# Kernel tuning notes

Hardware: AMD Instinct MI355X
Metric: run time of the kernel (lower is better)

Reference implementation:

```python
import jax, jax.numpy as jnp
import numpy as np

N0, N1, N2 = 100000, 25000, 6250
E0, E1, E2 = 600000, 150000, 40000
K = 6
NUM_CLASSES = 10


def setup_inputs() -> dict:
    key = jax.random.key(0)
    ks = jax.random.split(key, 20)
    inp = {
        "pos": jax.random.normal(ks[0], (N0, 3), dtype=jnp.float32),
        "edge_index0": jax.random.randint(ks[1], (2, E0), 0, N0, dtype=jnp.int32),
        "edge_index1": jax.random.randint(ks[2], (2, E1), 0, N1, dtype=jnp.int32),
        "edge_index2": jax.random.randint(ks[3], (2, E2), 0, N2, dtype=jnp.int32),
        "d0_rows": jax.random.randint(ks[4], (N0,), 0, N1, dtype=jnp.int32),
        "d0_cols": jax.random.randint(ks[5], (N0,), 0, N0, dtype=jnp.int32),
        "d0_vals": jax.random.uniform(ks[6], (N0,), dtype=jnp.float32),
        "d1_rows": jax.random.randint(ks[7], (N1,), 0, N2, dtype=jnp.int32),
        "d1_cols": jax.random.randint(ks[8], (N1,), 0, N1, dtype=jnp.int32),
        "d1_vals": jax.random.uniform(ks[9], (N1,), dtype=jnp.float32),
        "W0": jax.random.normal(ks[10], (K, 3, 32), dtype=jnp.float32) * 0.1,
        "b0": jax.random.normal(ks[11], (32,), dtype=jnp.float32) * 0.1,
        "W1": jax.random.normal(ks[12], (K, 32, 64), dtype=jnp.float32) * 0.1,
        "b1": jax.random.normal(ks[13], (64,), dtype=jnp.float32) * 0.1,
        "W2": jax.random.normal(ks[14], (K, 64, 128), dtype=jnp.float32) * 0.1,
        "b2": jax.random.normal(ks[15], (128,), dtype=jnp.float32) * 0.1,
        "lin_w": jax.random.normal(ks[16], (NUM_CLASSES, N2 * 128), dtype=jnp.float32) * 0.01,
        "lin_b": jax.random.normal(ks[17], (NUM_CLASSES,), dtype=jnp.float32) * 0.1,
    }
    return inp


def _cheb_edge_weights(row, col, n):
    # PyG get_laplacian(sym) followed by 2L/lambda_max - I with lambda_max=2:
    # diagonal becomes 0, off-diagonal weight = -deg^{-1/2}[row] * deg^{-1/2}[col]
    deg = jax.ops.segment_sum(jnp.ones(row.shape[0], jnp.float32), row, num_segments=n)
    dinv = jnp.where(deg > 0, 1.0 / jnp.sqrt(deg), 0.0)
    return -dinv[row] * dinv[col]


def _cheb_conv(x, edge_index, W, b, n):
    # Chebyshev recurrence: Tx0 = x, Tx1 = L_hat x, Tx_k = 2 L_hat Tx_{k-1} - Tx_{k-2}
    row, col = edge_index[0], edge_index[1]
    w = _cheb_edge_weights(row, col, n)

    def prop(z):  # [n, C] -> [n, C] scatter-gather over edges
        return jax.ops.segment_sum(w[:, None] * z[col], row, num_segments=n)

    Tx0 = x
    out = Tx0 @ W[0]
    Tx1 = prop(x)
    out = out + Tx1 @ W[1]
    for k in range(2, W.shape[0]):
        Tx2 = 2.0 * prop(Tx1) - Tx0
        out = out + Tx2 @ W[k]
        Tx0, Tx1 = Tx1, Tx2
    return out + b


def _pool(x, rows, cols, vals, n_out):
    # torch.sparse.mm(D, x) with D given in COO form
    return jax.ops.segment_sum(vals[:, None] * x[cols], rows, num_segments=n_out)


def reference(pos, edge_index0, edge_index1, edge_index2,
              d0_rows, d0_cols, d0_vals, d1_rows, d1_cols, d1_vals,
              W0, b0, W1, b1, W2, b2, lin_w, lin_b):
    x = jax.nn.relu(_cheb_conv(pos, edge_index0, W0, b0, N0))
    x = _pool(x, d0_rows, d0_cols, d0_vals, N1)
    x = jax.nn.relu(_cheb_conv(x, edge_index1, W1, b1, N1))
    x = _pool(x, d1_rows, d1_cols, d1_vals, N2)
    x = _cheb_conv(x, edge_index2, W2, b2, N2)  # no ReLU on last conv
    Z = lin_w @ x.reshape(-1) + lin_b
    return Z
```

## Files before the change

kernel.cpp:

```cpp
#include <hip/hip_runtime.h>


#define TPB 256
#define NB   318
#define BCAP 8192
#define EPB  4096
#define TXS  800000LL

static inline int gs(long long n) { return (int)((n + TPB - 1) / TPB); }

struct Desc5 {
    const int* rows[5];
    const int* cols[5];
    const float* vals[5];
    int eoff[6];
    int doff[5];
};


__global__ void k_binA(Desc5 d, int* __restrict__ gbcnt, int2* __restrict__ binrec,
                       int Etot) {
    __shared__ int2 srec[EPB];
    __shared__ unsigned short sbuck[EPB];
    __shared__ int scnt[NB], sbase[NB], slcur[NB];
    int tid = threadIdx.x;
    int e0 = blockIdx.x * EPB;
    int ne = min(EPB, Etot - e0);
    for (int b = tid; b < NB; b += 256) scnt[b] = 0;
    __syncthreads();
    for (int i = tid; i < ne; i += 256) {
        int e = e0 + i;
        int s = 0;
        while (e >= d.eoff[s + 1]) ++s;
        int le = e - d.eoff[s];
        int grow = d.doff[s] + d.rows[s][le];
        int col = d.cols[s][le];
        int vb = (s >= 3) ? __float_as_int(d.vals[s][le]) : 0;
        int b = grow >> 9;
        srec[i] = make_int2(((grow & 511) << 17) | col, vb);
        sbuck[i] = (unsigned short)b;
        atomicAdd(&scnt[b], 1);
    }
    __syncthreads();
    for (int b = tid; b < NB; b += 256) {
        sbase[b] = scnt[b] > 0 ? atomicAdd(&gbcnt[b], scnt[b]) : 0;
        slcur[b] = 0;
    }
    __syncthreads();
    for (int i = tid; i < ne; i += 256) {
        int b = sbuck[i];
        int off = atomicAdd(&slcur[b], 1);
        binrec[(long long)b * BCAP + sbase[b] + off] = srec[i];
    }
}

__global__ void k_bscan(const int* __restrict__ gbcnt, int* __restrict__ gbbase) {
    int lane = threadIdx.x;
    int carry = 0;
    for (int base = 0; base < NB; base += 64) {
        int i = base + lane;
        int v = (i < NB) ? gbcnt[i] : 0;
        int s = v;
#pragma unroll
        for (int off = 1; off < 64; off <<= 1) {
            int t = __shfl_up(s, off, 64);
            if (lane >= off) s += t;
        }
        if (i < NB) gbbase[i] = carry + s - v;
        carry += __shfl(s, 63, 64);
    }
}

__global__ void k_B1(const int* __restrict__ gbcnt, const int* __restrict__ gbbase,
                     const int2* __restrict__ binrec, int* __restrict__ rowptr,
                     float* __restrict__ dinv, int ntot, int ndinv, int Etot) {
    __shared__ int cnt[512], lexcl[512], wsum[4];
    int bucket = blockIdx.x, tid = threadIdx.x;
    int ne = gbcnt[bucket];
    const int2* br = binrec + (long long)bucket * BCAP;
    cnt[2 * tid] = 0; cnt[2 * tid + 1] = 0;
    __syncthreads();
    for (int i = tid; i < ne; i += 256)
        atomicAdd(&cnt[br[i].x >> 17], 1);
    __syncthreads();
    int c0 = cnt[2 * tid], c1 = cnt[2 * tid + 1], p = c0 + c1;
    int lane = tid & 63, wid = tid >> 6;
    int s = p;
#pragma unroll
    for (int off = 1; off < 64; off <<= 1) {
        int t = __shfl_up(s, off, 64);
        if (lane >= off) s += t;
    }
    if (lane == 63) wsum[wid] = s;
    __syncthreads();
    int add = 0;
    for (int w = 0; w < wid; ++w) add += wsum[w];
    int ep = add + s - p;
    lexcl[2 * tid] = ep; lexcl[2 * tid + 1] = ep + c0;
    __syncthreads();
    int base = gbbase[bucket];
    int row0 = bucket << 9;
    int nrows = min(512, ntot - row0);
    for (int lr = tid; lr < nrows; lr += 256) {
        int grow = row0 + lr;
        rowptr[grow] = base + lexcl[lr];
        if (grow < ndinv) {
            int c = cnt[lr];
            dinv[grow] = c > 0 ? 1.0f / sqrtf((float)c) : 0.f;
        }
    }
    if (bucket == 0 && tid == 0) rowptr[ntot] = Etot;
}

__global__ void k_B2(const int* __restrict__ gbcnt, const int2* __restrict__ binrec,
                     const int* __restrict__ rowptr, const float* __restrict__ dinv,
                     int2* __restrict__ rec, int ntot) {
    __shared__ int lbase[512], lcur[512];
    int bucket = blockIdx.x, tid = threadIdx.x;
    int row0 = bucket << 9;
    for (int i = tid; i < 512; i += 256) {
        int grow = row0 + i;
        lbase[i] = (grow < ntot) ? rowptr[grow] : 0;
        lcur[i] = 0;
    }
    __syncthreads();
    int ne = gbcnt[bucket];
    const int2* br = binrec + (long long)bucket * BCAP;
    for (int i = tid; i < ne; i += 256) {
        int2 r = br[i];
        int lr = r.x >> 17, col = r.x & 0x1FFFF;
        int grow = row0 + lr;
        int pos = lbase[lr] + atomicAdd(&lcur[lr], 1);
        float wv;
        if (grow < 100000)      wv = dinv[col];
        else if (grow < 125000) wv = dinv[100000 + col];
        else if (grow < 131250) wv = dinv[125000 + col];
        else                    wv = __int_as_float(r.y);
        rec[pos] = make_int2(col, __float_as_int(wv));
    }
}

__global__ void k_pad4(const float* __restrict__ pos, float4* __restrict__ dst, int n) {
    int i = blockIdx.x * blockDim.x + threadIdx.x;
    if (i < n) dst[i] = make_float4(pos[3 * i], pos[3 * i + 1], pos[3 * i + 2], 0.f);
}


__global__ void k_sprop_c4(const int* __restrict__ rowptr, const int2* __restrict__ rec,
                           const float* __restrict__ dinv, const float* __restrict__ src,
                           const float* __restrict__ prev, float* __restrict__ dst,
                           int n, int mode) {
    int r = blockIdx.x * blockDim.x + threadIdx.x;
    if (r >= n) return;
    int s0 = rowptr[r], s1 = rowptr[r + 1];
    float4 a0 = make_float4(0.f, 0.f, 0.f, 0.f);
    float4 a1 = a0, a2 = a0, a3 = a0;
    int j = s0;
    if ((j & 1) && j < s1) {
        int2 rr = rec[j];
        float w = __int_as_float(rr.y);
        float4 s = *(const float4*)(src + (long long)rr.x * 4);
        a0.x += w * s.x; a0.y += w * s.y; a0.z += w * s.z; a0.w += w * s.w;
        ++j;
    }
    for (; j + 4 <= s1; j += 4) {
        int4 q0 = *(const int4*)(rec + j);
        int4 q1 = *(const int4*)(rec + j + 2);
        float w0 = __int_as_float(q0.y), w1 = __int_as_float(q0.w);
        float w2 = __int_as_float(q1.y), w3 = __int_as_float(q1.w);
        float4 s0v = *(const float4*)(src + (long long)q0.x * 4);
        float4 s1v = *(const float4*)(src + (long long)q0.z * 4);
        float4 s2v = *(const float4*)(src + (long long)q1.x * 4);
        float4 s3v = *(const float4*)(src + (long long)q1.z * 4);
        a0.x += w0 * s0v.x; a0.y += w0 * s0v.y; a0.z += w0 * s0v.z; a0.w += w0 * s0v.w;
        a1.x += w1 * s1v.x; a1.y += w1 * s1v.y; a1.z += w1 * s1v.z; a1.w += w1 * s1v.w;
        a2.x += w2 * s2v.x; a2.y += w2 * s2v.y; a2.z += w2 * s2v.z; a2.w += w2 * s2v.w;
        a3.x += w3 * s3v.x; a3.y += w3 * s3v.y; a3.z += w3 * s3v.z; a3.w += w3 * s3v.w;
    }
    if (j + 2 <= s1) {
        int4 q = *(const int4*)(rec + j);
        float wa = __int_as_float(q.y), wb = __int_as_float(q.w);
        float4 sa = *(const float4*)(src + (long long)q.x * 4);
        float4 sb = *(const float4*)(src + (long long)q.z * 4);
        a0.x += wa * sa.x; a0.y += wa * sa.y; a0.z += wa * sa.z; a0.w += wa * sa.w;
        a1.x += wb * sb.x; a1.y += wb * sb.y; a1.z += wb * sb.z; a1.w += wb * sb.w;
        j += 2;
    }
    if (j < s1) {
        int2 rr = rec[j];
        float w = __int_as_float(rr.y);
        float4 s = *(const float4*)(src + (long long)rr.x * 4);
        a0.x += w * s.x; a0.y += w * s.y; a0.z += w * s.z; a0.w += w * s.w;
    }
    a0.x += a1.x + a2.x + a3.x; a0.y += a1.y + a2.y + a3.y;
    a0.z += a1.z + a2.z + a3.z; a0.w += a1.w + a2.w + a3.w;
    float m = -dinv[r];
    long long o = (long long)r * 4;
    float4 out;
    if (mode) {
        float4 p = *(const float4*)(prev + o);
        out.x = 2.f * m * a0.x - p.x; out.y = 2.f * m * a0.y - p.y;
        out.z = 2.f * m * a0.z - p.z; out.w = 2.f * m * a0.w - p.w;
    } else {
        out.x = m * a0.x; out.y = m * a0.y; out.z = m * a0.z; out.w = m * a0.w;
    }
    *(float4*)(dst + o) = out;
}

__global__ __launch_bounds__(256, 4)
void k_conv0_final(const int* __restrict__ rowptr, const int2* __restrict__ rec,
                   const float* __restrict__ dinv, const float* __restrict__ txbase,
                   const float* __restrict__ W, const float* __restrict__ b,
                   float* __restrict__ out, int n) {
    int r = blockIdx.x * blockDim.x + threadIdx.x;
    if (r >= n) return;
    const float* src = txbase + 4 * TXS;
    int s0 = rowptr[r], s1 = rowptr[r + 1];
    float4 a0 = make_float4(0.f, 0.f, 0.f, 0.f);
    float4 a1 = a0;
    int j = s0;
    if ((j & 1) && j < s1) {
        int2 rr = rec[j];
        float w = __int_as_float(rr.y);
        float4 s = *(const float4*)(src + (long long)rr.x * 4);
        a0.x += w * s.x; a0.y += w * s.y; a0.z += w * s.z;
        ++j;
    }
    for (; j + 2 <= s1; j += 2) {
        int4 q = *(const int4*)(rec + j);
        float wa = __int_as_float(q.y), wb = __int_as_float(q.w);
        float4 sa = *(const float4*)(src + (long long)q.x * 4);
        float4 sb = *(const float4*)(src + (long long)q.z * 4);
        a0.x += wa * sa.x; a0.y += wa * sa.y; a0.z += wa * sa.z;
        a1.x += wb * sb.x; a1.y += wb * sb.y; a1.z += wb * sb.z;
    }
    if (j < s1) {
        int2 rr = rec[j];
        float w = __int_as_float(rr.y);
        float4 s = *(const float4*)(src + (long long)rr.x * 4);
        a0.x += w * s.x; a0.y += w * s.y; a0.z += w * s.z;
    }
    a0.x += a1.x; a0.y += a1.y; a0.z += a1.z;
    float m = -dinv[r];
    float4 xv[6];
#pragma unroll
    for (int k = 0; k < 5; ++k)
        xv[k] = *(const float4*)(txbase + (long long)k * TXS + (long long)r * 4);
    xv[5].x = 2.f * m * a0.x - xv[3].x;
    xv[5].y = 2.f * m * a0.y - xv[3].y;
    xv[5].z = 2.f * m * a0.z - xv[3].z;
    float* op = out + (long long)r * 32;
#pragma unroll 1
    for (int co4 = 0; co4 < 8; ++co4) {
        float4 acc = *(const float4*)(b + co4 * 4);
#pragma unroll
        for (int k = 0; k < 6; ++k) {
            const float* Wk = W + k * 96 + co4 * 4;
            float4 w0 = *(const float4*)(Wk);
            float4 w1 = *(const float4*)(Wk + 32);
            float4 w2 = *(const float4*)(Wk + 64);
            acc.x += xv[k].x * w0.x + xv[k].y * w1.x + xv[k].z * w2.x;
            acc.y += xv[k].x * w0.y + xv[k].y * w1.y + xv[k].z * w2.y;
            acc.z += xv[k].x * w0.z + xv[k].y * w1.z + xv[k].z * w2.z;
            acc.w += xv[k].x * w0.w + xv[k].y * w1.w + xv[k].z * w2.w;
        }
        *(float4*)(op + co4 * 4) = acc;
    }
}

template <int C>
__global__ void k_sprop_t(const int* __restrict__ rowptr, const int2* __restrict__ rec,
                          const float* __restrict__ dinv, const float* __restrict__ src,
                          const float* __restrict__ prev, float* __restrict__ dst,
                          int n, int mode) {
    constexpr int C4 = C / 4;
    int idx = blockIdx.x * blockDim.x + threadIdx.x;
    if (idx >= n * C4) return;
    int r = idx / C4, c4 = (idx - r * C4) * 4;
    int s0 = rowptr[r], s1 = rowptr[r + 1];
    float4 acca = make_float4(0.f, 0.f, 0.f, 0.f);
    float4 accb = make_float4(0.f, 0.f, 0.f, 0.f);
    int j = s0;
    if ((j & 1) && j < s1) {
        int2 rr = rec[j];
        float w = __int_as_float(rr.y);
        float4 s = *(const float4*)(src + (long long)rr.x * C + c4);
        acca.x += w * s.x; acca.y += w * s.y; acca.z += w * s.z; acca.w += w * s.w;
        ++j;
    }
    for (; j + 2 <= s1; j += 2) {
        int4 q = *(const int4*)(rec + j);
        float wa = __int_as_float(q.y), wb = __int_as_float(q.w);
        float4 sa = *(const float4*)(src + (long long)q.x * C + c4);
        float4 sb = *(const float4*)(src + (long long)q.z * C + c4);
        acca.x += wa * sa.x; acca.y += wa * sa.y; acca.z += wa * sa.z; acca.w += wa * sa.w;
        accb.x += wb * sb.x; accb.y += wb * sb.y; accb.z += wb * sb.z; accb.w += wb * sb.w;
    }
    if (j < s1) {
        int2 rr = rec[j];
        float w = __int_as_float(rr.y);
        float4 s = *(const float4*)(src + (long long)rr.x * C + c4);
        acca.x += w * s.x; acca.y += w * s.y; acca.z += w * s.z; acca.w += w * s.w;
    }
    acca.x += accb.x; acca.y += accb.y; acca.z += accb.z; acca.w += accb.w;
    float m = -dinv[r];
    long long o = (long long)r * C + c4;
    float4 out;
    if (mode) {
        float4 p = *(const float4*)(prev + o);
        out.x = 2.f * m * acca.x - p.x; out.y = 2.f * m * acca.y - p.y;
        out.z = 2.f * m * acca.z - p.z; out.w = 2.f * m * acca.w - p.w;
    } else {
        out.x = m * acca.x; out.y = m * acca.y; out.z = m * acca.z; out.w = m * acca.w;
    }
    *(float4*)(dst + o) = out;
}


template <int C>
__global__ void k_spool4_t(const int* __restrict__ rowptr, const int2* __restrict__ rec,
                           const float* __restrict__ x, float* __restrict__ out, int n) {
    constexpr int C4 = C / 4;
    int idx = blockIdx.x * blockDim.x + threadIdx.x;
    if (idx >= n * C4) return;
    int r = idx / C4, c4 = (idx - r * C4) * 4;
    int s0 = rowptr[r], s1 = rowptr[r + 1];
    float4 acca = make_float4(0.f, 0.f, 0.f, 0.f);
    float4 accb = make_float4(0.f, 0.f, 0.f, 0.f);
    int j = s0;
    if ((j & 1) && j < s1) {
        int2 rr = rec[j];
        float v = __int_as_float(rr.y);
        float4 s = *(const float4*)(x + (long long)rr.x * C + c4);
        acca.x += v * fmaxf(s.x, 0.f); acca.y += v * fmaxf(s.y, 0.f);
        acca.z += v * fmaxf(s.z, 0.f); acca.w += v * fmaxf(s.w, 0.f);
        ++j;
    }
    for (; j + 2 <= s1; j += 2) {
        int4 q = *(const int4*)(rec + j);
        float va = __int_as_float(q.y), vb = __int_as_float(q.w);
        float4 sa = *(const float4*)(x + (long long)q.x * C + c4);
        float4 sb = *(const float4*)(x + (long long)q.z * C + c4);
        acca.x += va * fmaxf(sa.x, 0.f); acca.y += va * fmaxf(sa.y, 0.f);
        acca.z += va * fmaxf(sa.z, 0.f); acca.w += va * fmaxf(sa.w, 0.f);
        accb.x += vb * fmaxf(sb.x, 0.f); accb.y += vb * fmaxf(sb.y, 0.f);
        accb.z += vb * fmaxf(sb.z, 0.f); accb.w += vb * fmaxf(sb.w, 0.f);
    }
    if (j < s1) {
        int2 rr = rec[j];
        float v = __int_as_float(rr.y);
        float4 s = *(const float4*)(x + (long long)rr.x * C + c4);
        acca.x += v * fmaxf(s.x, 0.f); acca.y += v * fmaxf(s.y, 0.f);
        acca.z += v * fmaxf(s.z, 0.f); acca.w += v * fmaxf(s.w, 0.f);
    }
    acca.x += accb.x; acca.y += accb.y; acca.z += accb.z; acca.w += accb.w;
    *(float4*)(out + (long long)r * C + c4) = acca;
}


template <int C, int KSPLIT>
__global__ void k_pool_f(const int* __restrict__ rowptr, const int2* __restrict__ rec,
                         const float* __restrict__ part, const float* __restrict__ bias,
                         float* __restrict__ out, int n, int partStride) {
    constexpr int C4 = C / 4;
    int idx = blockIdx.x * blockDim.x + threadIdx.x;
    if (idx >= n * C4) return;
    int r = idx / C4, c4 = (idx - r * C4) * 4;
    int s0 = rowptr[r], s1 = rowptr[r + 1];
    float4 bb = *(const float4*)(bias + c4);
    float4 acc = make_float4(0.f, 0.f, 0.f, 0.f);
    for (int j = s0; j < s1; ++j) {
        int2 rr = rec[j];
        float v = __int_as_float(rr.y);
        float4 x = bb;
#pragma unroll
        for (int s = 0; s < KSPLIT; ++s) {
            float4 p = *(const float4*)(part + (long long)s * partStride + (long long)rr.x * C + c4);
            x.x += p.x; x.y += p.y; x.z += p.z; x.w += p.w;
        }
        acc.x += v * fmaxf(x.x, 0.f); acc.y += v * fmaxf(x.y, 0.f);
        acc.z += v * fmaxf(x.z, 0.f); acc.w += v * fmaxf(x.w, 0.f);
    }
    *(float4*)(out + (long long)r * C + c4) = acc;
}


template <int CIN, int COUT, int KSPLIT, int NT>
__global__ __launch_bounds__(256, 4)
void k_outsplit4(float* __restrict__ part, const float* __restrict__ txbase,
                 const float* __restrict__ W, int n, int partStride) {
    constexpr int CO4 = COUT / 4;
    constexpr int KPER = 6 / KSPLIT;
    int per = (n / NT) * CO4;
    int idx = blockIdx.x * blockDim.x + threadIdx.x;
    if (idx >= per * KSPLIT) return;
    int s = idx / per, t = idx - s * per;
    int tile = t / CO4, co = (t - tile * CO4) * 4;
    int node0 = tile * NT;
    float4 acc[NT];
#pragma unroll
    for (int i = 0; i < NT; ++i) acc[i] = make_float4(0.f, 0.f, 0.f, 0.f);
#pragma unroll 1
    for (int kk = 0; kk < KPER; ++kk) {
        int k = s * KPER + kk;
        const float* xb = txbase + (long long)k * TXS + (long long)node0 * CIN;
        const float* Wk = W + (long long)k * CIN * COUT + co;
#pragma unroll 1
        for (int c4 = 0; c4 < CIN / 4; ++c4) {
            const float* Wr = Wk + c4 * 4 * COUT;
            float4 w0 = *(const float4*)(Wr);
            float4 w1 = *(const float4*)(Wr + COUT);
            float4 w2 = *(const float4*)(Wr + 2 * COUT);
            float4 w3 = *(const float4*)(Wr + 3 * COUT);
#pragma unroll
            for (int i = 0; i < NT; ++i) {
                float4 xv = *(const float4*)(xb + i * CIN + c4 * 4);
                acc[i].x += xv.x * w0.x + xv.y * w1.x + xv.z * w2.x + xv.w * w3.x;
                acc[i].y += xv.x * w0.y + xv.y * w1.y + xv.z * w2.y + xv.w * w3.y;
                acc[i].z += xv.x * w0.z + xv.y * w1.z + xv.z * w2.z + xv.w * w3.z;
                acc[i].w += xv.x * w0.w + xv.y * w1.w + xv.z * w2.w + xv.w * w3.w;
            }
        }
    }
    float* op = part + (long long)s * partStride + (long long)node0 * COUT + co;
#pragma unroll
    for (int i = 0; i < NT; ++i)
        *(float4*)(op + (long long)i * COUT) = acc[i];
}


__global__ void k_linear_partial_f(const float* __restrict__ lw,
                                   const float4* __restrict__ part,
                                   const float* __restrict__ b2,
                                   float* __restrict__ partials,
                                   int len4, int len, int nblk) {
    float acc[10];
#pragma unroll
    for (int j = 0; j < 10; ++j) acc[j] = 0.f;
    const float4* b2v = (const float4*)b2;
    for (int i = blockIdx.x * blockDim.x + threadIdx.x; i < len4;
         i += gridDim.x * blockDim.x) {
        float4 xv = b2v[i & 31];
#pragma unroll
        for (int s = 0; s < 6; ++s) {
            float4 p = part[s * 200000 + i];
            xv.x += p.x; xv.y += p.y; xv.z += p.z; xv.w += p.w;
        }
#pragma unroll
        for (int j = 0; j < 10; ++j) {
            float4 wv = *(const float4*)(lw + (long long)j * len + i * 4);
            acc[j] += xv.x * wv.x + xv.y * wv.y + xv.z * wv.z + xv.w * wv.w;
        }
    }
    __shared__ float lds[4][10];
    int wid = threadIdx.x >> 6, lane = threadIdx.x & 63;
#pragma unroll
    for (int j = 0; j < 10; ++j) {
        float v = acc[j];
        for (int off = 32; off > 0; off >>= 1) v += __shfl_down(v, off, 64);
        if (lane == 0) lds[wid][j] = v;
    }
    __syncthreads();
    if (threadIdx.x < 10) {
        float s = lds[0][threadIdx.x] + lds[1][threadIdx.x] +
                  lds[2][threadIdx.x] + lds[3][threadIdx.x];
        partials[threadIdx.x * nblk + blockIdx.x] = s;
    }
}

__global__ void k_linear_final(const float* __restrict__ partials,
                               const float* __restrict__ lb,
                               float* __restrict__ out, int nblk) {
    int j = threadIdx.x >> 6, lane = threadIdx.x & 63;
    float v = 0.f;
    for (int b = lane; b < nblk; b += 64) v += partials[j * nblk + b];
    for (int off = 32; off > 0; off >>= 1) v += __shfl_down(v, off, 64);
    if (lane == 0) out[j] = lb[j] + v;
}

extern "C" void kernel_launch(void* const* d_in, const int* in_sizes, int n_in,
                              void* d_out, int out_size, void* d_ws, size_t ws_size,
                              hipStream_t stream) {
    const int cN0 = 100000, cN1 = 25000, cN2 = 6250;
    const int cE0 = 600000, cE1 = 150000, cE2 = 40000;
    const int NBLK = 512;

    const float* pos = (const float*)d_in[0];
    const int*   ei0 = (const int*)d_in[1];
    const int*   ei1 = (const int*)d_in[2];
    const int*   ei2 = (const int*)d_in[3];
    const int*   d0r = (const int*)d_in[4];
    const int*   d0c = (const int*)d_in[5];
    const float* d0v = (const float*)d_in[6];
    const int*   d1r = (const int*)d_in[7];
    const int*   d1c = (const int*)d_in[8];
    const float* d1v = (const float*)d_in[9];
    const float* W0  = (const float*)d_in[10];
    const float* b0  = (const float*)d_in[11];
    const float* W1  = (const float*)d_in[12];
    const float* b1  = (const float*)d_in[13];
    const float* W2  = (const float*)d_in[14];
    const float* b2  = (const float*)d_in[15];
    const float* lw  = (const float*)d_in[16];
    const float* lb  = (const float*)d_in[17];
    float* outZ = (float*)d_out;

    const int ntot = cN0 + cN1 + cN2 + cN1 + cN2;
    const int Etot = cE0 + cE1 + cE2 + cN0 + cN1;
    const int Eg   = cE0 + cE1 + cE2;
    const int ndinv = cN0 + cN1 + cN2;
    const int doff0 = 0, doff1 = cN0, doff2 = cN0 + cN1,
              doffp0 = doff2 + cN2, doffp1 = doffp0 + cN1;

    int*   iws    = (int*)d_ws;
    int*   gbcnt  = iws;
    int*   gbbase = gbcnt + 320;
    int*   rowptr = gbbase + 320;
    float* dinv   = (float*)(rowptr + 162504);
    int2*  binrec = (int2*)(dinv + 131256);
    int2*  rec    = binrec + (long long)NB * BCAP;
    float* txbuf  = (float*)(rec + 915000);
    float* part   = txbuf + 6 * TXS;
    float* bufOut = part + 4800000;
    float* lpart  = bufOut + 3200000;

    Desc5 d;
    d.rows[0] = ei0;        d.cols[0] = ei0 + cE0; d.vals[0] = nullptr;
    d.rows[1] = ei1;        d.cols[1] = ei1 + cE1; d.vals[1] = nullptr;
    d.rows[2] = ei2;        d.cols[2] = ei2 + cE2; d.vals[2] = nullptr;
    d.rows[3] = d0r;        d.cols[3] = d0c;       d.vals[3] = d0v;
    d.rows[4] = d1r;        d.cols[4] = d1c;       d.vals[4] = d1v;
    d.eoff[0] = 0;
    d.eoff[1] = cE0;
    d.eoff[2] = cE0 + cE1;
    d.eoff[3] = Eg;
    d.eoff[4] = Eg + cN0;
    d.eoff[5] = Etot;
    d.doff[0] = doff0; d.doff[1] = doff1; d.doff[2] = doff2;
    d.doff[3] = doffp0; d.doff[4] = doffp1;

    k_pad4<<<gs(cN0), TPB, 0, stream>>>(pos, (float4*)txbuf, cN0);

    hipMemsetAsync(gbcnt, 0, (size_t)NB * 4, stream);
    k_binA<<<(Etot + EPB - 1) / EPB, TPB, 0, stream>>>(d, gbcnt, binrec, Etot);
    k_bscan<<<1, 64, 0, stream>>>(gbcnt, gbbase);
    k_B1<<<NB, TPB, 0, stream>>>(gbcnt, gbbase, binrec, rowptr, dinv, ntot, ndinv, Etot);
    k_B2<<<NB, TPB, 0, stream>>>(gbcnt, binrec, rowptr, dinv, rec, ntot);

    auto run_sprops = [&](int doffs, int n, int Cs, int kmax) {
        const int* rp = rowptr + doffs;
        const float* dv = dinv + doffs;
        auto sprop = [&](int kdst, int mode) {
            const float* src = txbuf + (long long)(kdst - 1) * TXS;
            const float* prev = (kdst >= 2) ? txbuf + (long long)(kdst - 2) * TXS : nullptr;
            float* dst = txbuf + (long long)kdst * TXS;
            long long work = (long long)n * (Cs >> 2);
            if (Cs == 4)
                k_sprop_c4<<<gs(n), TPB, 0, stream>>>(rp, rec, dv, src, prev, dst, n, mode);
            else if (Cs == 32)
                k_sprop_t<32><<<gs(work), TPB, 0, stream>>>(rp, rec, dv, src, prev, dst, n, mode);
            else
                k_sprop_t<64><<<gs(work), TPB, 0, stream>>>(rp, rec, dv, src, prev, dst, n, mode);
        };
        sprop(1, 0);
        for (int k = 2; k <= kmax; ++k) sprop(k, 1);
    };

    run_sprops(doff0, cN0, 4, 4);
    k_conv0_final<<<gs(cN0), TPB, 0, stream>>>(
        rowptr + doff0, rec, dinv + doff0, txbuf, W0, b0, bufOut, cN0);
    k_spool4_t<32><<<gs((long long)cN1 * 8), TPB, 0, stream>>>(
        rowptr + doffp0, rec, bufOut, txbuf, cN1);

    run_sprops(doff1, cN1, 32, 5);
    {
        const int pstride = cN1 * 64;
        k_outsplit4<32, 64, 3, 4><<<gs((long long)(cN1 / 4) * 16 * 3), TPB, 0, stream>>>(
            part, txbuf, W1, cN1, pstride);
        k_pool_f<64, 3><<<gs((long long)cN2 * 16), TPB, 0, stream>>>(
            rowptr + doffp1, rec, part, b1, txbuf, cN2, pstride);
    }

    run_sprops(doff2, cN2, 64, 5);
    {
        const int pstride = cN2 * 128;
        k_outsplit4<64, 128, 6, 2><<<gs((long long)(cN2 / 2) * 32 * 6), TPB, 0, stream>>>(
            part, txbuf, W2, cN2, pstride);
        k_linear_partial_f<<<NBLK, TPB, 0, stream>>>(
            lw, (const float4*)part, b2, lpart, cN2 * 128 / 4, cN2 * 128, NBLK);
        k_linear_final<<<1, 640, 0, stream>>>(lpart, lb, outZ, NBLK);
    }
}
```

Baseline: 269.0 us.

## Fuse Chebyshev propagation chains into persistent cooperative kernels with grid sync

Replaces the per-order sparse propagation launches (4-5 per conv layer) with one cooperative kernel per layer. The kernel uses a grid-stride loop and grid.sync between Chebyshev orders. This removes launch overhead and inter-kernel gaps for the small layers. In exchange the grid is capped at 1024 blocks and each order pays a grid barrier, which may reduce latency hiding for the large 100k-node layer.

```diff
diff --git a/kernel.cpp b/kernel.cpp
--- a/kernel.cpp
+++ b/kernel.cpp
@@ -1,4 +1,5 @@
 #include <hip/hip_runtime.h>
+#include <hip/hip_cooperative_groups.h>
 
 
 #define TPB 256
@@ -146,65 +147,86 @@
 }
 
 
-__global__ void k_sprop_c4(const int* __restrict__ rowptr, const int2* __restrict__ rec,
-                           const float* __restrict__ dinv, const float* __restrict__ src,
-                           const float* __restrict__ prev, float* __restrict__ dst,
-                           int n, int mode) {
-    int r = blockIdx.x * blockDim.x + threadIdx.x;
-    if (r >= n) return;
-    int s0 = rowptr[r], s1 = rowptr[r + 1];
-    float4 a0 = make_float4(0.f, 0.f, 0.f, 0.f);
-    float4 a1 = a0, a2 = a0, a3 = a0;
-    int j = s0;
-    if ((j & 1) && j < s1) {
-        int2 rr = rec[j];
-        float w = __int_as_float(rr.y);
-        float4 s = *(const float4*)(src + (long long)rr.x * 4);
-        a0.x += w * s.x; a0.y += w * s.y; a0.z += w * s.z; a0.w += w * s.w;
-        ++j;
-    }
-    for (; j + 4 <= s1; j += 4) {
-        int4 q0 = *(const int4*)(rec + j);
-        int4 q1 = *(const int4*)(rec + j + 2);
-        float w0 = __int_as_float(q0.y), w1 = __int_as_float(q0.w);
-        float w2 = __int_as_float(q1.y), w3 = __int_as_float(q1.w);
-        float4 s0v = *(const float4*)(src + (long long)q0.x * 4);
-        float4 s1v = *(const float4*)(src + (long long)q0.z * 4);
-        float4 s2v = *(const float4*)(src + (long long)q1.x * 4);
-        float4 s3v = *(const float4*)(src + (long long)q1.z * 4);
-        a0.x += w0 * s0v.x; a0.y += w0 * s0v.y; a0.z += w0 * s0v.z; a0.w += w0 * s0v.w;
-        a1.x += w1 * s1v.x; a1.y += w1 * s1v.y; a1.z += w1 * s1v.z; a1.w += w1 * s1v.w;
-        a2.x += w2 * s2v.x; a2.y += w2 * s2v.y; a2.z += w2 * s2v.z; a2.w += w2 * s2v.w;
-        a3.x += w3 * s3v.x; a3.y += w3 * s3v.y; a3.z += w3 * s3v.z; a3.w += w3 * s3v.w;
-    }
-    if (j + 2 <= s1) {
-        int4 q = *(const int4*)(rec + j);
-        float wa = __int_as_float(q.y), wb = __int_as_float(q.w);
-        float4 sa = *(const float4*)(src + (long long)q.x * 4);
-        float4 sb = *(const float4*)(src + (long long)q.z * 4);
-        a0.x += wa * sa.x; a0.y += wa * sa.y; a0.z += wa * sa.z; a0.w += wa * sa.w;
-        a1.x += wb * sb.x; a1.y += wb * sb.y; a1.z += wb * sb.z; a1.w += wb * sb.w;
-        j += 2;
-    }
-    if (j < s1) {
-        int2 rr = rec[j];
-        float w = __int_as_float(rr.y);
-        float4 s = *(const float4*)(src + (long long)rr.x * 4);
-        a0.x += w * s.x; a0.y += w * s.y; a0.z += w * s.z; a0.w += w * s.w;
-    }
-    a0.x += a1.x + a2.x + a3.x; a0.y += a1.y + a2.y + a3.y;
-    a0.z += a1.z + a2.z + a3.z; a0.w += a1.w + a2.w + a3.w;
-    float m = -dinv[r];
-    long long o = (long long)r * 4;
-    float4 out;
-    if (mode) {
-        float4 p = *(const float4*)(prev + o);
-        out.x = 2.f * m * a0.x - p.x; out.y = 2.f * m * a0.y - p.y;
-        out.z = 2.f * m * a0.z - p.z; out.w = 2.f * m * a0.w - p.w;
-    } else {
-        out.x = m * a0.x; out.y = m * a0.y; out.z = m * a0.z; out.w = m * a0.w;
-    }
-    *(float4*)(dst + o) = out;
+template <int C>
+__global__ __launch_bounds__(256, 4)
+void k_sprop_chain(const int* __restrict__ rowptr, const int2* __restrict__ rec,
+                   const float* __restrict__ dinv, float* __restrict__ txbuf,
+                   int n, int kmax) {
+    namespace cg = cooperative_groups;
+    cg::grid_group grid = cg::this_grid();
+    constexpr int C4 = C / 4;
+    int total = n * C4;
+    int stride = gridDim.x * blockDim.x;
+    int tid0 = blockIdx.x * blockDim.x + threadIdx.x;
+    for (int k = 1; k <= kmax; ++k) {
+        const float* src = txbuf + (long long)(k - 1) * TXS;
+        const float* prev = txbuf + (long long)(k >= 2 ? k - 2 : 0) * TXS;
+        float* dst = txbuf + (long long)k * TXS;
+        bool m1 = (k >= 2);
+        for (int idx = tid0; idx < total; idx += stride) {
+            int r, c4;
+            if constexpr (C4 == 1) { r = idx; c4 = 0; }
+            else { r = idx / C4; c4 = (idx - r * C4) * 4; }
+            int s0 = rowptr[r], s1 = rowptr[r + 1];
+            float4 a0 = make_float4(0.f, 0.f, 0.f, 0.f);
+            float4 a1 = a0;
+            int j = s0;
+            if ((j & 1) && j < s1) {
+                int2 rr = rec[j];
+                float w = __int_as_float(rr.y);
+                float4 s = *(const float4*)(src + (long long)rr.x * C + c4);
+                a0.x += w * s.x; a0.y += w * s.y; a0.z += w * s.z; a0.w += w * s.w;
+                ++j;
+            }
+            if constexpr (C4 == 1) {
+                float4 a2 = make_float4(0.f, 0.f, 0.f, 0.f);
+                float4 a3 = a2;
+                for (; j + 4 <= s1; j += 4) {
+                    int4 q0 = *(const int4*)(rec + j);
+                    int4 q1 = *(const int4*)(rec + j + 2);
+                    float w0 = __int_as_float(q0.y), w1 = __int_as_float(q0.w);
+                    float w2 = __int_as_float(q1.y), w3 = __int_as_float(q1.w);
+                    float4 s0v = *(const float4*)(src + (long long)q0.x * 4);
+                    float4 s1v = *(const float4*)(src + (long long)q0.z * 4);
+                    float4 s2v = *(const float4*)(src + (long long)q1.x * 4);
+                    float4 s3v = *(const float4*)(src + (long long)q1.z * 4);
+                    a0.x += w0 * s0v.x; a0.y += w0 * s0v.y; a0.z += w0 * s0v.z; a0.w += w0 * s0v.w;
+                    a1.x += w1 * s1v.x; a1.y += w1 * s1v.y; a1.z += w1 * s1v.z; a1.w += w1 * s1v.w;
+                    a2.x += w2 * s2v.x; a2.y += w2 * s2v.y; a2.z += w2 * s2v.z; a2.w += w2 * s2v.w;
+                    a3.x += w3 * s3v.x; a3.y += w3 * s3v.y; a3.z += w3 * s3v.z; a3.w += w3 * s3v.w;
+                }
+                a0.x += a2.x + a3.x; a0.y += a2.y + a3.y;
+                a0.z += a2.z + a3.z; a0.w += a2.w + a3.w;
+            }
+            for (; j + 2 <= s1; j += 2) {
+                int4 q = *(const int4*)(rec + j);
+                float wa = __int_as_float(q.y), wb = __int_as_float(q.w);
+                float4 sa = *(const float4*)(src + (long long)q.x * C + c4);
+                float4 sb = *(const float4*)(src + (long long)q.z * C + c4);
+                a0.x += wa * sa.x; a0.y += wa * sa.y; a0.z += wa * sa.z; a0.w += wa * sa.w;
+                a1.x += wb * sb.x; a1.y += wb * sb.y; a1.z += wb * sb.z; a1.w += wb * sb.w;
+            }
+            if (j < s1) {
+                int2 rr = rec[j];
+                float w = __int_as_float(rr.y);
+                float4 s = *(const float4*)(src + (long long)rr.x * C + c4);
+                a0.x += w * s.x; a0.y += w * s.y; a0.z += w * s.z; a0.w += w * s.w;
+            }
+            a0.x += a1.x; a0.y += a1.y; a0.z += a1.z; a0.w += a1.w;
+            float m = -dinv[r];
+            long long o = (long long)r * C + c4;
+            float4 out;
+            if (m1) {
+                float4 p = *(const float4*)(prev + o);
+                out.x = 2.f * m * a0.x - p.x; out.y = 2.f * m * a0.y - p.y;
+                out.z = 2.f * m * a0.z - p.z; out.w = 2.f * m * a0.w - p.w;
+            } else {
+                out.x = m * a0.x; out.y = m * a0.y; out.z = m * a0.z; out.w = m * a0.w;
+            }
+            *(float4*)(dst + o) = out;
+        }
+        if (k < kmax) grid.sync();
+    }
 }
 
 __global__ __launch_bounds__(256, 4)
@@ -266,54 +288,6 @@
         }
         *(float4*)(op + co4 * 4) = acc;
     }
-}
-
-template <int C>
-__global__ void k_sprop_t(const int* __restrict__ rowptr, const int2* __restrict__ rec,
-                          const float* __restrict__ dinv, const float* __restrict__ src,
-                          const float* __restrict__ prev, float* __restrict__ dst,
-                          int n, int mode) {
-    constexpr int C4 = C / 4;
-    int idx = blockIdx.x * blockDim.x + threadIdx.x;
-    if (idx >= n * C4) return;
-    int r = idx / C4, c4 = (idx - r * C4) * 4;
-    int s0 = rowptr[r], s1 = rowptr[r + 1];
-    float4 acca = make_float4(0.f, 0.f, 0.f, 0.f);
-    float4 accb = make_float4(0.f, 0.f, 0.f, 0.f);
-    int j = s0;
-    if ((j & 1) && j < s1) {
-        int2 rr = rec[j];
-        float w = __int_as_float(rr.y);
-        float4 s = *(const float4*)(src + (long long)rr.x * C + c4);
-        acca.x += w * s.x; acca.y += w * s.y; acca.z += w * s.z; acca.w += w * s.w;
-        ++j;
-    }
-    for (; j + 2 <= s1; j += 2) {
-        int4 q = *(const int4*)(rec + j);
-        float wa = __int_as_float(q.y), wb = __int_as_float(q.w);
-        float4 sa = *(const float4*)(src + (long long)q.x * C + c4);
-        float4 sb = *(const float4*)(src + (long long)q.z * C + c4);
-        acca.x += wa * sa.x; acca.y += wa * sa.y; acca.z += wa * sa.z; acca.w += wa * sa.w;
-        accb.x += wb * sb.x; accb.y += wb * sb.y; accb.z += wb * sb.z; accb.w += wb * sb.w;
-    }
-    if (j < s1) {
-        int2 rr = rec[j];
-        float w = __int_as_float(rr.y);
-        float4 s = *(const float4*)(src + (long long)rr.x * C + c4);
-        acca.x += w * s.x; acca.y += w * s.y; acca.z += w * s.z; acca.w += w * s.w;
-    }
-    acca.x += accb.x; acca.y += accb.y; acca.z += accb.z; acca.w += accb.w;
-    float m = -dinv[r];
-    long long o = (long long)r * C + c4;
-    float4 out;
-    if (mode) {
-        float4 p = *(const float4*)(prev + o);
-        out.x = 2.f * m * acca.x - p.x; out.y = 2.f * m * acca.y - p.y;
-        out.z = 2.f * m * acca.z - p.z; out.w = 2.f * m * acca.w - p.w;
-    } else {
-        out.x = m * acca.x; out.y = m * acca.y; out.z = m * acca.z; out.w = m * acca.w;
-    }
-    *(float4*)(dst + o) = out;
 }
 
 
@@ -547,32 +521,37 @@
     k_B1<<<NB, TPB, 0, stream>>>(gbcnt, gbbase, binrec, rowptr, dinv, ntot, ndinv, Etot);
     k_B2<<<NB, TPB, 0, stream>>>(gbcnt, binrec, rowptr, dinv, rec, ntot);
 
-    auto run_sprops = [&](int doffs, int n, int Cs, int kmax) {
+    auto launch_chain = [&](int doffs, int n, int Cs, int kmax) {
         const int* rp = rowptr + doffs;
         const float* dv = dinv + doffs;
-        auto sprop = [&](int kdst, int mode) {
-            const float* src = txbuf + (long long)(kdst - 1) * TXS;
-            const float* prev = (kdst >= 2) ? txbuf + (long long)(kdst - 2) * TXS : nullptr;
-            float* dst = txbuf + (long long)kdst * TXS;
-            long long work = (long long)n * (Cs >> 2);
-            if (Cs == 4)
-                k_sprop_c4<<<gs(n), TPB, 0, stream>>>(rp, rec, dv, src, prev, dst, n, mode);
-            else if (Cs == 32)
-                k_sprop_t<32><<<gs(work), TPB, 0, stream>>>(rp, rec, dv, src, prev, dst, n, mode);
-            else
-                k_sprop_t<64><<<gs(work), TPB, 0, stream>>>(rp, rec, dv, src, prev, dst, n, mode);
-        };
-        sprop(1, 0);
-        for (int k = 2; k <= kmax; ++k) sprop(k, 1);
+        int total = n * (Cs / 4);
+        int nb = (total + TPB - 1) / TPB;
+        if (nb > 1024) nb = 1024;
+        void* args[6];
+        args[0] = (void*)&rp;
+        args[1] = (void*)&rec;
+        args[2] = (void*)&dv;
+        args[3] = (void*)&txbuf;
+        args[4] = (void*)&n;
+        args[5] = (void*)&kmax;
+        if (Cs == 4)
+            hipLaunchCooperativeKernel(reinterpret_cast<void*>(&k_sprop_chain<4>),
+                                       dim3(nb), dim3(TPB), args, 0, stream);
+        else if (Cs == 32)
+            hipLaunchCooperativeKernel(reinterpret_cast<void*>(&k_sprop_chain<32>),
+                                       dim3(nb), dim3(TPB), args, 0, stream);
+        else
+            hipLaunchCooperativeKernel(reinterpret_cast<void*>(&k_sprop_chain<64>),
+                                       dim3(nb), dim3(TPB), args, 0, stream);
     };
 
-    run_sprops(doff0, cN0, 4, 4);
+    launch_chain(doff0, cN0, 4, 4);
     k_conv0_final<<<gs(cN0), TPB, 0, stream>>>(
         rowptr + doff0, rec, dinv + doff0, txbuf, W0, b0, bufOut, cN0);
     k_spool4_t<32><<<gs((long long)cN1 * 8), TPB, 0, stream>>>(
         rowptr + doffp0, rec, bufOut, txbuf, cN1);
 
-    run_sprops(doff1, cN1, 32, 5);
+    launch_chain(doff1, cN1, 32, 5);
     {
         const int pstride = cN1 * 64;
         k_outsplit4<32, 64, 3, 4><<<gs((long long)(cN1 / 4) * 16 * 3), TPB, 0, stream>>>(
@@ -581,7 +560,7 @@
             rowptr + doffp1, rec, part, b1, txbuf, cN2, pstride);
     }
 
-    run_sprops(doff2, cN2, 64, 5);
+    launch_chain(doff2, cN2, 64, 5);
     {
         const int pstride = cN2 * 128;
         k_outsplit4<64, 128, 6, 2><<<gs((long long)(cN2 / 2) * 32 * 6), TPB, 0, stream>>>(
```

Result: slower. 988.6 us (+267.5%).
